# Kernel optimization log

Measured on AMD Instinct MI355X. Metric: run time of the kernel, lower is better.

Reference implementation:

```python
import jax, jax.numpy as jnp
import numpy as np
from jax import lax

V_PATCH_NUMS = (1, 2, 4, 8, 16)
BETA = 0.25
QUANT_RESI = 0.5
NUM_PHI = 4  # share_quant_resi=4 -> PhiPartiallyShared

# PhiPartiallyShared tick lookup (K=4 -> linspace(1/12, 11/12, 4))
def _phi_indices():
    K = NUM_PHI
    ticks = np.linspace(1/3/K, 1 - 1/3/K, K) if K == 4 else np.linspace(1/2/K, 1 - 1/2/K, K)
    SN = len(V_PATCH_NUMS)
    return [int(np.argmin(np.abs(ticks - si/(SN-1)))) for si in range(SN)]

PHI_IDX = _phi_indices()  # [0, 1, 1, 2, 3]


def phi_apply(h, w, b, ratio=QUANT_RESI):
    # h_out = (1-a)*h + a*Conv3x3(h), padding=1
    conv = lax.conv_general_dilated(h, w, (1, 1), 'SAME',
                                    dimension_numbers=('NCHW', 'OIHW', 'NCHW'))
    conv = conv + b[None, :, None, None]
    return h * (1.0 - ratio) + conv * ratio


def vq_forward(f_BChw, emb_w, phi_w, phi_b):
    f = f_BChw.astype(jnp.float32)
    B, C, H, W = f.shape
    f_ng = lax.stop_gradient(f)
    f_rest = f_ng
    f_hat = jnp.zeros_like(f)
    SN = len(V_PATCH_NUMS)
    loss = jnp.float32(0.0)
    emb_ng = lax.stop_gradient(emb_w)  # distances use .data (no grad)
    e_sq = jnp.sum(emb_ng * emb_ng, axis=1)  # [V]
    for si, pn in enumerate(V_PATCH_NUMS):
        if si != SN - 1:
            k = H // pn  # exact area pooling (divisible sizes)
            z = f_rest.reshape(B, C, pn, k, pn, k).mean(axis=(3, 5))
        else:
            z = f_rest
        z_NC = z.transpose(0, 2, 3, 1).reshape(-1, C)  # [B*pn*pn, C]
        # squared L2 distance to every code, argmin
        d = (jnp.sum(z_NC * z_NC, axis=1, keepdims=True) + e_sq
             - 2.0 * z_NC @ emb_ng.T)  # [N, V]
        idx = jnp.argmin(d, axis=1)  # [N]
        h = emb_w[idx].reshape(B, pn, pn, C).transpose(0, 3, 1, 2)  # [B,C,pn,pn]
        if si != SN - 1:
            h = jax.image.resize(h, (B, C, H, W), method='cubic')  # bicubic upsample
        pi = PHI_IDX[si]
        h = phi_apply(h, phi_w[pi], phi_b[pi])
        f_hat = f_hat + h
        f_rest = f_rest - h
        loss = loss + (BETA * jnp.mean((lax.stop_gradient(f_hat) - f) ** 2)
                       + jnp.mean((f_hat - f_ng) ** 2))
    loss = loss / SN
    # straight-through estimator
    f_hat_out = lax.stop_gradient(f_hat) - f_ng + f
    return f_hat_out, loss


def setup_inputs() -> dict:
    key = jax.random.key(0)
    k1, k2, k3 = jax.random.split(key, 3)
    B, C, H, W = 64, 32, 16, 16
    V = 4096
    f_BChw = jax.random.normal(k1, (B, C, H, W), dtype=jnp.float32)
    emb_w = jax.random.normal(k2, (V, C), dtype=jnp.float32) * 0.5
    phi_w = jax.random.normal(k3, (NUM_PHI, C, C, 3, 3), dtype=jnp.float32) * 0.05
    phi_b = jnp.zeros((NUM_PHI, C), dtype=jnp.float32)
    return {'f_BChw': f_BChw, 'emb_w': emb_w, 'phi_w': phi_w, 'phi_b': phi_b}


def reference(f_BChw, emb_w, phi_w, phi_b):
    return vq_forward(f_BChw, emb_w, phi_w, phi_b)
```

## Files before the change

kernel.cpp:

```cpp
#include <hip/hip_runtime.h>

typedef unsigned long long u64;

#define B_ 64
#define C_ 32
#define H_ 16
#define W_ 16
#define V_ 4096
#define NELEM_ (B_*C_*H_*W_)
#define NPOS_TOTAL 21824


__device__ __forceinline__ float keys_cubic(float x) {
  if (x >= 2.f) return 0.f;
  if (x >= 1.f) return ((-0.5f*x + 2.5f)*x - 4.f)*x + 2.f;
  return (1.5f*x - 2.5f)*x*x + 1.f;
}

__device__ __forceinline__ u64 pack_key(float d, int idx) {
  unsigned bu = __float_as_uint(d);
  unsigned m = bu ^ ((bu >> 31) ? 0xFFFFFFFFu : 0x80000000u);
  return ((u64)m << 32) | (unsigned)idx;
}


__global__ void setup_kernel(const float* __restrict__ f, const float* __restrict__ emb,
                             float* __restrict__ e_sq, u64* __restrict__ part,
                             float* __restrict__ z0) {
  int i = blockIdx.x*blockDim.x + threadIdx.x;
  if (i < NPOS_TOTAL) part[i] = ~0ull;
  if (i < V_) {
    const float4* p = (const float4*)(emb + (size_t)i*32);
    float s = 0.f;
#pragma unroll
    for (int j = 0; j < 8; ++j) { float4 q = p[j]; s += q.x*q.x + q.y*q.y + q.z*q.z + q.w*q.w; }
    e_sq[i] = s;
  }
  if (i < B_*C_) {
    const float4* p = (const float4*)(f + (size_t)i*256);
    float s = 0.f;
    for (int j = 0; j < 64; ++j) { float4 q = p[j]; s += (q.x + q.y) + (q.z + q.w); }
    z0[i] = s * (1.f/256.f);
  }
}


template<int P, int TILE>
__global__ void __launch_bounds__(256, 2) argmin2_kernel(
    const float* __restrict__ z, const float* __restrict__ emb,
    const float* __restrict__ e_sq, u64* __restrict__ part, int cpc) {
  __shared__ float cl[TILE*32];
  __shared__ float es[TILE];
  const int tid = threadIdx.x;
  const int n0 = blockIdx.x*(256*P) + tid;
  float zb[P][32]; float zz[P];
#pragma unroll
  for (int p = 0; p < P; ++p) {
    const float4* zp = (const float4*)(z + (size_t)(n0 + p*256)*32);
#pragma unroll
    for (int i = 0; i < 8; ++i) {
      float4 q = zp[i];
      zb[p][4*i+0]=q.x; zb[p][4*i+1]=q.y; zb[p][4*i+2]=q.z; zb[p][4*i+3]=q.w;
    }
    float s = 0.f;
#pragma unroll
    for (int i = 0; i < 32; ++i) s = fmaf(zb[p][i], zb[p][i], s);
    zz[p] = s;
  }
  const int v0 = blockIdx.y * cpc;
  float bd[P]; int bi[P];
#pragma unroll
  for (int p = 0; p < P; ++p) { bd[p] = 3.4e38f; bi[p] = v0; }
  for (int t0 = 0; t0 < cpc; t0 += TILE) {
    __syncthreads();
    const float4* src = (const float4*)(emb + (size_t)(v0 + t0)*32);
    for (int e = tid; e < TILE*8; e += 256) ((float4*)cl)[e] = src[e];
    if (tid < TILE) es[tid] = e_sq[v0 + t0 + tid];
    __syncthreads();
#pragma unroll 2
    for (int c = 0; c < TILE; ++c) {
      const float4* cp = (const float4*)(cl + c*32);
      float4 q[8];
#pragma unroll
      for (int i = 0; i < 8; ++i) q[i] = cp[i];
      float ev = es[c];
#pragma unroll
      for (int p = 0; p < P; ++p) {
        float a0=0.f, a1=0.f, a2=0.f, a3=0.f;
#pragma unroll
        for (int i = 0; i < 8; ++i) {
          a0 = fmaf(zb[p][4*i+0], q[i].x, a0);
          a1 = fmaf(zb[p][4*i+1], q[i].y, a1);
          a2 = fmaf(zb[p][4*i+2], q[i].z, a2);
          a3 = fmaf(zb[p][4*i+3], q[i].w, a3);
        }
        float dot = (a0+a1)+(a2+a3);
        float d = (zz[p] + ev) - 2.f*dot;
        bool lt = d < bd[p];
        bd[p] = lt ? d : bd[p];
        bi[p] = lt ? (v0 + t0 + c) : bi[p];
      }
    }
  }
#pragma unroll
  for (int p = 0; p < P; ++p)
    atomicMin(part + n0 + p*256, pack_key(bd[p], bi[p]));
}

__global__ void __launch_bounds__(256) argmin0_kernel(
    const float* __restrict__ z, const float* __restrict__ emb,
    const float* __restrict__ e_sq, u64* __restrict__ part) {
  __shared__ float cl[64*32];
  __shared__ float es[64];
  const int tid = threadIdx.x;
  const int v0 = blockIdx.x * 64;
  const float4* src = (const float4*)(emb + (size_t)v0*32);
  for (int e = tid; e < 64*8; e += 256) ((float4*)cl)[e] = src[e];
  if (tid < 64) es[tid] = e_sq[v0 + tid];
  __syncthreads();
  const int p = tid & 63, sub = tid >> 6;
  float zb[32];
  const float4* zp = (const float4*)(z + (size_t)p*32);
#pragma unroll
  for (int i = 0; i < 8; ++i) {
    float4 q = zp[i];
    zb[4*i+0]=q.x; zb[4*i+1]=q.y; zb[4*i+2]=q.z; zb[4*i+3]=q.w;
  }
  float zz = 0.f;
#pragma unroll
  for (int i = 0; i < 32; ++i) zz = fmaf(zb[i], zb[i], zz);
  float bd = 3.4e38f; int bi = v0;
  for (int c = sub*16; c < sub*16 + 16; ++c) {
    const float4* cp = (const float4*)(cl + c*32);
    float4 q[8];
#pragma unroll
    for (int i = 0; i < 8; ++i) q[i] = cp[i];
    float a0=0.f, a1=0.f, a2=0.f, a3=0.f;
#pragma unroll
    for (int i = 0; i < 8; ++i) {
      a0 = fmaf(zb[4*i+0], q[i].x, a0);
      a1 = fmaf(zb[4*i+1], q[i].y, a1);
      a2 = fmaf(zb[4*i+2], q[i].z, a2);
      a3 = fmaf(zb[4*i+3], q[i].w, a3);
    }
    float dot = (a0+a1)+(a2+a3);
    float d = (zz + es[c]) - 2.f*dot;
    if (d < bd) { bd = d; bi = v0 + c; }
  }
  atomicMin(part + p, pack_key(bd, bi));
}


template<int PN, int NEXT_PN, bool FIRST>
__global__ void __launch_bounds__(512) upconv_kernel(
    const u64* __restrict__ part_s,
    const float* __restrict__ emb,
    const float* __restrict__ phi_w,
    const float* __restrict__ phi_b,
    const float* __restrict__ f,
    float* __restrict__ f_hat,
    float* __restrict__ f_rest,
    float* __restrict__ z_next,
    float* __restrict__ loss_part)
{
  constexpr int PN2 = PN*PN;
  constexpr bool POOLED = (NEXT_PN != 0 && NEXT_PN < 16);
  const int b = blockIdx.x;
  const int cg = blockIdx.y;
  const int tid = threadIdx.x;

  __shared__ int   idx_s[PN2];
  __shared__ float W4[16][4];
  __shared__ int   I0[16];
  __shared__ float tmp_s[(PN < 16) ? C_*PN*16 : 1];
  __shared__ float pool_s[POOLED ? 8*256 : 1];
  union HupHs { float hup[C_*16*18]; float hs[C_*16*18]; };
  __shared__ HupHs u;
  __shared__ float wsum[8];

  for (int p = tid; p < PN2; p += 512)
    idx_s[p] = (int)(part_s[b*PN2 + p] & 0xFFFFFFFFull);

  if (PN < 16 && tid < 16) {
    float sf = (tid + 0.5f) * ((float)PN/16.f) - 0.5f;
    int i0 = (int)floorf(sf) - 1;
    float w[4]; float tot = 0.f;
#pragma unroll
    for (int t = 0; t < 4; ++t) {
      int i = i0 + t;
      float wv = (i >= 0 && i < PN) ? keys_cubic(fabsf(sf - (float)i)) : 0.f;
      w[t] = wv; tot += wv;
    }
    float r = 1.f/tot;
#pragma unroll
    for (int t = 0; t < 4; ++t) W4[tid][t] = w[t]*r;
    I0[tid] = i0;
  }
  __syncthreads();

  if (PN < 16) {
    for (int e = tid; e < C_*PN2; e += 512) {
      int c = e / PN2, p = e % PN2;
      u.hs[c*PN2 + p] = emb[(size_t)idx_s[p]*32 + c];
    }
  } else {
    for (int e = tid; e < C_*256; e += 512) {
      int c = e >> 8, p = e & 255;
      int y = p >> 4, x = p & 15;
      u.hup[(c*16 + y)*18 + 1 + x] = emb[(size_t)idx_s[p]*32 + c];
    }
    for (int e = tid; e < C_*16; e += 512) { u.hup[e*18] = 0.f; u.hup[e*18 + 17] = 0.f; }
  }
  __syncthreads();

  if (PN < 16) {
    for (int e = tid; e < C_*PN*16; e += 512) {
      int jx = e & 15; int rest = e >> 4;
      int iy = rest % PN; int c = rest / PN;
      int i0 = I0[jx];
      float s = 0.f;
#pragma unroll
      for (int t = 0; t < 4; ++t) {
        int ix = i0 + t; int ixc = min(max(ix, 0), PN-1);
        s += W4[jx][t] * u.hs[(c*PN + iy)*PN + ixc];
      }
      tmp_s[(c*PN + iy)*16 + jx] = s;
    }
    __syncthreads();
    for (int e = tid; e < C_*16; e += 512) { u.hup[e*18] = 0.f; u.hup[e*18 + 17] = 0.f; }
    for (int e = tid; e < C_*256; e += 512) {
      int jx = e & 15; int jy = (e >> 4) & 15; int c = e >> 8;
      int i0 = I0[jy];
      float s = 0.f;
#pragma unroll
      for (int t = 0; t < 4; ++t) {
        int iy = i0 + t; int iyc = min(max(iy, 0), PN-1);
        s += W4[jy][t] * tmp_s[(c*PN + iyc)*16 + jx];
      }
      u.hup[(c*16 + jy)*18 + 1 + jx] = s;
    }
    __syncthreads();
  }

  const int px = tid & 255;
  const int g  = tid >> 8;
  const int y  = px >> 4, x = px & 15;
  const int co0 = cg*8 + g*4;
  const float* wbase = phi_w + (size_t)co0*32*9;
  float acc[4];
#pragma unroll
  for (int o = 0; o < 4; ++o) acc[o] = phi_b[co0 + o];
  for (int ci = 0; ci < 32; ++ci) {
    float wn[9];
#pragma unroll
    for (int ky = 0; ky < 3; ++ky) {
      int yy = y + ky - 1;
      bool v = (yy >= 0 && yy <= 15);
      const float* r = &u.hup[(ci*16 + (v ? yy : 0))*18 + x];
      wn[ky*3+0] = v ? r[0] : 0.f;
      wn[ky*3+1] = v ? r[1] : 0.f;
      wn[ky*3+2] = v ? r[2] : 0.f;
    }
#pragma unroll
    for (int o = 0; o < 4; ++o) {
      const float* wp = wbase + ((size_t)o*32 + ci)*9;
#pragma unroll
      for (int t = 0; t < 9; ++t) acc[o] = fmaf(wp[t], wn[t], acc[o]);
    }
  }

  float lsum = 0.f;
#pragma unroll
  for (int o = 0; o < 4; ++o) {
    int co = co0 + o;
    float hv = 0.5f*u.hup[(co*16 + y)*18 + 1 + x] + 0.5f*acc[o];
    size_t gi = (((size_t)b*C_ + co)*16 + y)*16 + x;
    float fv = f[gi];
    float fh = FIRST ? hv : (f_hat[gi] + hv);
    f_hat[gi] = fh;
    if constexpr (NEXT_PN != 0) {
      float nfr = FIRST ? (fv - hv) : (f_rest[gi] - hv);
      f_rest[gi] = nfr;
      if constexpr (NEXT_PN == 16) {
        z_next[((size_t)b*256 + px)*32 + co] = nfr;
      } else {
        pool_s[(g*4 + o)*256 + px] = nfr;
      }
    }
    float dd = fh - fv;
    lsum = fmaf(dd, dd, lsum);
  }
  if constexpr (POOLED) {
    constexpr int NP = (NEXT_PN > 0) ? NEXT_PN : 1;
    constexpr int NP2 = NP*NP;
    constexpr int KP = 16/NP;
    __syncthreads();
    if (tid < 8*NP2) {
      int c_l = tid / NP2, p = tid % NP2;
      int yy = (p / NP)*KP, xx = (p % NP)*KP;
      float s = 0.f;
      for (int a = 0; a < KP; ++a)
        for (int e = 0; e < KP; ++e)
          s += pool_s[c_l*256 + (yy + a)*16 + xx + e];
      z_next[((size_t)b*NP2 + p)*32 + cg*8 + c_l] = s * (1.f/(float)(KP*KP));
    }
  }
#pragma unroll
  for (int off = 32; off > 0; off >>= 1) lsum += __shfl_down(lsum, off);
  if ((tid & 63) == 0) wsum[tid >> 6] = lsum;
  __syncthreads();
  if (tid == 0) {
    float s = 0.f;
#pragma unroll
    for (int i = 0; i < 8; ++i) s += wsum[i];
    loss_part[blockIdx.y*64 + blockIdx.x] = s;
  }
}

__global__ void loss_kernel(const float* __restrict__ loss_part, float* __restrict__ out_loss) {
  __shared__ float s[256];
  int t = threadIdx.x;
  float v = 0.f;
#pragma unroll
  for (int i = 0; i < 5; ++i) v += loss_part[i*256 + t];
  s[t] = v;
  __syncthreads();
  for (int off = 128; off > 0; off >>= 1) {
    if (t < off) s[t] += s[t + off];
    __syncthreads();
  }
  if (t == 0) out_loss[0] = s[0] * (1.25f / (5.f * (float)NELEM_));
}


extern "C" void kernel_launch(void* const* d_in, const int* in_sizes, int n_in,
                              void* d_out, int out_size, void* d_ws, size_t ws_size,
                              hipStream_t stream) {
  const float* f     = (const float*)d_in[0];
  const float* emb   = (const float*)d_in[1];
  const float* phi_w = (const float*)d_in[2];
  const float* phi_b = (const float*)d_in[3];
  float* f_hat    = (float*)d_out;
  float* out_loss = f_hat + NELEM_;

  char* ws = (char*)d_ws;
  float* f_rest = (float*)ws;
  float* z      = f_rest + NELEM_;
  u64*   part   = (u64*)(z + NELEM_);
  float* e_sq   = (float*)(part + NPOS_TOTAL);
  float* loss_part = e_sq + V_;

  const float* pw0 = phi_w;                 const float* pb0 = phi_b;
  const float* pw1 = phi_w + 1*32*32*9;     const float* pb1 = phi_b + 1*32;
  const float* pw2 = phi_w + 2*32*32*9;     const float* pb2 = phi_b + 2*32;
  const float* pw3 = phi_w + 3*32*32*9;     const float* pb3 = phi_b + 3*32;

  setup_kernel<<<(NPOS_TOTAL + 255)/256, 256, 0, stream>>>(f, emb, e_sq, part, z);

  dim3 cgrid(B_, 4);
  argmin0_kernel<<<64, 256, 0, stream>>>(z, emb, e_sq, part + 0);
  upconv_kernel<1, 2, true><<<cgrid, 512, 0, stream>>>(part + 0, emb, pw0, pb0,
      f, f_hat, f_rest, z, loss_part + 0*256);
  argmin2_kernel<1,16><<<dim3(1,256), 256, 0, stream>>>(z, emb, e_sq, part + 64, 16);
  upconv_kernel<2, 4, false><<<cgrid, 512, 0, stream>>>(part + 64, emb, pw1, pb1,
      f, f_hat, f_rest, z, loss_part + 1*256);
  argmin2_kernel<2,32><<<dim3(2,128), 256, 0, stream>>>(z, emb, e_sq, part + 320, 32);
  upconv_kernel<4, 8, false><<<cgrid, 512, 0, stream>>>(part + 320, emb, pw2, pb2,
      f, f_hat, f_rest, z, loss_part + 2*256);
  argmin2_kernel<4,64><<<dim3(4,64), 256, 0, stream>>>(z, emb, e_sq, part + 1344, 64);
  upconv_kernel<8, 16, false><<<cgrid, 512, 0, stream>>>(part + 1344, emb, pw2, pb2,
      f, f_hat, f_rest, z, loss_part + 3*256);
  argmin2_kernel<4,64><<<dim3(16,32), 256, 0, stream>>>(z, emb, e_sq, part + 5440, 128);
  upconv_kernel<16, 0, false><<<cgrid, 512, 0, stream>>>(part + 5440, emb, pw3, pb3,
      f, f_hat, f_rest, z, loss_part + 4*256);

  loss_kernel<<<1, 256, 0, stream>>>(loss_part, out_loss);
}
```

Before: 240.2 us.

## Replace atomicMin argmin with per-chunk partial keys reduced in upconv

The argmin kernels no longer stage codebook tiles in shared memory. Each thread streams code vectors straight from global memory with double-buffered register prefetch. Instead of atomicMin into a pre-cleared buffer, each codebook chunk writes its own partial key, and the following upconv kernel reduces across chunks. This removes the init pass, the atomics and the block barriers, at the cost of larger partial buffers and a serial reduction loop in upconv. The partial buffers reuse the f_rest workspace, which is safe only because f_rest is no longer written in the last pre-final stage. Grid shapes are retuned per stage.

```diff
diff --git a/kernel.cpp b/kernel.cpp
--- a/kernel.cpp
+++ b/kernel.cpp
@@ -4,11 +4,8 @@
 
 #define B_ 64
 #define C_ 32
-#define H_ 16
-#define W_ 16
 #define V_ 4096
-#define NELEM_ (B_*C_*H_*W_)
-#define NPOS_TOTAL 21824
+#define NELEM_ (B_*C_*16*16)
 
 
 __device__ __forceinline__ float keys_cubic(float x) {
@@ -25,10 +22,8 @@
 
 
 __global__ void setup_kernel(const float* __restrict__ f, const float* __restrict__ emb,
-                             float* __restrict__ e_sq, u64* __restrict__ part,
-                             float* __restrict__ z0) {
+                             float* __restrict__ e_sq, float* __restrict__ z0) {
   int i = blockIdx.x*blockDim.x + threadIdx.x;
-  if (i < NPOS_TOTAL) part[i] = ~0ull;
   if (i < V_) {
     const float4* p = (const float4*)(emb + (size_t)i*32);
     float s = 0.f;
@@ -45,12 +40,11 @@
 }
 
 
-template<int P, int TILE>
-__global__ void __launch_bounds__(256, 2) argmin2_kernel(
+template<int P>
+__global__ void __launch_bounds__(256) argmin_kernel(
     const float* __restrict__ z, const float* __restrict__ emb,
-    const float* __restrict__ e_sq, u64* __restrict__ part, int cpc) {
-  __shared__ float cl[TILE*32];
-  __shared__ float es[TILE];
+    const float* __restrict__ e_sq, u64* __restrict__ part_lo,
+    u64* __restrict__ part_hi, int split, int N, int cpc) {
   const int tid = threadIdx.x;
   const int n0 = blockIdx.x*(256*P) + tid;
   float zb[P][32]; float zz[P];
@@ -71,89 +65,148 @@
   float bd[P]; int bi[P];
 #pragma unroll
   for (int p = 0; p < P; ++p) { bd[p] = 3.4e38f; bi[p] = v0; }
-  for (int t0 = 0; t0 < cpc; t0 += TILE) {
-    __syncthreads();
-    const float4* src = (const float4*)(emb + (size_t)(v0 + t0)*32);
-    for (int e = tid; e < TILE*8; e += 256) ((float4*)cl)[e] = src[e];
-    if (tid < TILE) es[tid] = e_sq[v0 + t0 + tid];
-    __syncthreads();
-#pragma unroll 2
-    for (int c = 0; c < TILE; ++c) {
-      const float4* cp = (const float4*)(cl + c*32);
-      float4 q[8];
-#pragma unroll
-      for (int i = 0; i < 8; ++i) q[i] = cp[i];
-      float ev = es[c];
-#pragma unroll
-      for (int p = 0; p < P; ++p) {
-        float a0=0.f, a1=0.f, a2=0.f, a3=0.f;
-#pragma unroll
-        for (int i = 0; i < 8; ++i) {
-          a0 = fmaf(zb[p][4*i+0], q[i].x, a0);
-          a1 = fmaf(zb[p][4*i+1], q[i].y, a1);
-          a2 = fmaf(zb[p][4*i+2], q[i].z, a2);
-          a3 = fmaf(zb[p][4*i+3], q[i].w, a3);
-        }
-        float dot = (a0+a1)+(a2+a3);
-        float d = (zz[p] + ev) - 2.f*dot;
-        bool lt = d < bd[p];
-        bd[p] = lt ? d : bd[p];
-        bi[p] = lt ? (v0 + t0 + c) : bi[p];
-      }
-    }
-  }
-#pragma unroll
-  for (int p = 0; p < P; ++p)
-    atomicMin(part + n0 + p*256, pack_key(bd[p], bi[p]));
+
+  float4 qa[8], qb[8];
+  {
+    const float4* e4 = (const float4*)(emb + (size_t)v0*32);
+#pragma unroll
+    for (int i = 0; i < 8; ++i) qa[i] = e4[i];
+  }
+  for (int c = 0; c < cpc; c += 2) {
+    const int v = v0 + c;
+    {
+      const float4* en = (const float4*)(emb + (size_t)(v+1)*32);
+#pragma unroll
+      for (int i = 0; i < 8; ++i) qb[i] = en[i];
+    }
+    float ev = e_sq[v];
+#pragma unroll
+    for (int p = 0; p < P; ++p) {
+      float a0=0.f,a1=0.f,a2=0.f,a3=0.f;
+#pragma unroll
+      for (int i = 0; i < 8; ++i) {
+        a0 = fmaf(zb[p][4*i+0], qa[i].x, a0);
+        a1 = fmaf(zb[p][4*i+1], qa[i].y, a1);
+        a2 = fmaf(zb[p][4*i+2], qa[i].z, a2);
+        a3 = fmaf(zb[p][4*i+3], qa[i].w, a3);
+      }
+      float dot = (a0+a1)+(a2+a3);
+      float d = (zz[p] + ev) - 2.f*dot;
+      bool lt = d < bd[p];
+      bd[p] = lt ? d : bd[p];
+      bi[p] = lt ? v : bi[p];
+    }
+    int v2 = v + 2; if (v2 > V_-1) v2 = V_-1;
+    {
+      const float4* en = (const float4*)(emb + (size_t)v2*32);
+#pragma unroll
+      for (int i = 0; i < 8; ++i) qa[i] = en[i];
+    }
+    ev = e_sq[v+1];
+#pragma unroll
+    for (int p = 0; p < P; ++p) {
+      float a0=0.f,a1=0.f,a2=0.f,a3=0.f;
+#pragma unroll
+      for (int i = 0; i < 8; ++i) {
+        a0 = fmaf(zb[p][4*i+0], qb[i].x, a0);
+        a1 = fmaf(zb[p][4*i+1], qb[i].y, a1);
+        a2 = fmaf(zb[p][4*i+2], qb[i].z, a2);
+        a3 = fmaf(zb[p][4*i+3], qb[i].w, a3);
+      }
+      float dot = (a0+a1)+(a2+a3);
+      float d = (zz[p] + ev) - 2.f*dot;
+      bool lt = d < bd[p];
+      bd[p] = lt ? d : bd[p];
+      bi[p] = lt ? (v+1) : bi[p];
+    }
+  }
+  u64* pp = (blockIdx.y < split) ? (part_lo + (size_t)blockIdx.y*N)
+                                 : (part_hi + (size_t)(blockIdx.y - split)*N);
+#pragma unroll
+  for (int p = 0; p < P; ++p) pp[n0 + p*256] = pack_key(bd[p], bi[p]);
 }
 
 __global__ void __launch_bounds__(256) argmin0_kernel(
     const float* __restrict__ z, const float* __restrict__ emb,
-    const float* __restrict__ e_sq, u64* __restrict__ part) {
-  __shared__ float cl[64*32];
-  __shared__ float es[64];
-  const int tid = threadIdx.x;
-  const int v0 = blockIdx.x * 64;
-  const float4* src = (const float4*)(emb + (size_t)v0*32);
-  for (int e = tid; e < 64*8; e += 256) ((float4*)cl)[e] = src[e];
-  if (tid < 64) es[tid] = e_sq[v0 + tid];
+    const float* __restrict__ e_sq, u64* __restrict__ part_lo) {
+  __shared__ u64 wkey[4][64];
+  const int tid = threadIdx.x, lane = tid & 63;
+  const int w = __builtin_amdgcn_readfirstlane(tid >> 6);
+  float zb[32];
+  {
+    const float4* zp = (const float4*)(z + (size_t)lane*32);
+#pragma unroll
+    for (int i = 0; i < 8; ++i) {
+      float4 q = zp[i];
+      zb[4*i+0]=q.x; zb[4*i+1]=q.y; zb[4*i+2]=q.z; zb[4*i+3]=q.w;
+    }
+  }
+  float zz = 0.f;
+#pragma unroll
+  for (int i = 0; i < 32; ++i) zz = fmaf(zb[i], zb[i], zz);
+  const int v0 = blockIdx.x*256 + w*64;
+  float bd = 3.4e38f; int bi = v0;
+  float4 qa[8], qb[8];
+  {
+    const float4* e4 = (const float4*)(emb + (size_t)v0*32);
+#pragma unroll
+    for (int i = 0; i < 8; ++i) qa[i] = e4[i];
+  }
+  for (int c = 0; c < 64; c += 2) {
+    const int v = v0 + c;
+    {
+      const float4* en = (const float4*)(emb + (size_t)(v+1)*32);
+#pragma unroll
+      for (int i = 0; i < 8; ++i) qb[i] = en[i];
+    }
+    float ev = e_sq[v];
+    {
+      float a0=0.f,a1=0.f,a2=0.f,a3=0.f;
+#pragma unroll
+      for (int i = 0; i < 8; ++i) {
+        a0 = fmaf(zb[4*i+0], qa[i].x, a0);
+        a1 = fmaf(zb[4*i+1], qa[i].y, a1);
+        a2 = fmaf(zb[4*i+2], qa[i].z, a2);
+        a3 = fmaf(zb[4*i+3], qa[i].w, a3);
+      }
+      float d = (zz + ev) - 2.f*((a0+a1)+(a2+a3));
+      if (d < bd) { bd = d; bi = v; }
+    }
+    int v2 = v + 2; if (v2 > V_-1) v2 = V_-1;
+    {
+      const float4* en = (const float4*)(emb + (size_t)v2*32);
+#pragma unroll
+      for (int i = 0; i < 8; ++i) qa[i] = en[i];
+    }
+    ev = e_sq[v+1];
+    {
+      float a0=0.f,a1=0.f,a2=0.f,a3=0.f;
+#pragma unroll
+      for (int i = 0; i < 8; ++i) {
+        a0 = fmaf(zb[4*i+0], qb[i].x, a0);
+        a1 = fmaf(zb[4*i+1], qb[i].y, a1);
+        a2 = fmaf(zb[4*i+2], qb[i].z, a2);
+        a3 = fmaf(zb[4*i+3], qb[i].w, a3);
+      }
+      float d = (zz + ev) - 2.f*((a0+a1)+(a2+a3));
+      if (d < bd) { bd = d; bi = v+1; }
+    }
+  }
+  wkey[tid >> 6][lane] = pack_key(bd, bi);
   __syncthreads();
-  const int p = tid & 63, sub = tid >> 6;
-  float zb[32];
-  const float4* zp = (const float4*)(z + (size_t)p*32);
-#pragma unroll
-  for (int i = 0; i < 8; ++i) {
-    float4 q = zp[i];
-    zb[4*i+0]=q.x; zb[4*i+1]=q.y; zb[4*i+2]=q.z; zb[4*i+3]=q.w;
-  }
-  float zz = 0.f;
-#pragma unroll
-  for (int i = 0; i < 32; ++i) zz = fmaf(zb[i], zb[i], zz);
-  float bd = 3.4e38f; int bi = v0;
-  for (int c = sub*16; c < sub*16 + 16; ++c) {
-    const float4* cp = (const float4*)(cl + c*32);
-    float4 q[8];
-#pragma unroll
-    for (int i = 0; i < 8; ++i) q[i] = cp[i];
-    float a0=0.f, a1=0.f, a2=0.f, a3=0.f;
-#pragma unroll
-    for (int i = 0; i < 8; ++i) {
-      a0 = fmaf(zb[4*i+0], q[i].x, a0);
-      a1 = fmaf(zb[4*i+1], q[i].y, a1);
-      a2 = fmaf(zb[4*i+2], q[i].z, a2);
-      a3 = fmaf(zb[4*i+3], q[i].w, a3);
-    }
-    float dot = (a0+a1)+(a2+a3);
-    float d = (zz + es[c]) - 2.f*dot;
-    if (d < bd) { bd = d; bi = v0 + c; }
-  }
-  atomicMin(part + p, pack_key(bd, bi));
+  if (tid < 64) {
+    u64 best = wkey[0][tid];
+#pragma unroll
+    for (int ww = 1; ww < 4; ++ww) { u64 kk = wkey[ww][tid]; if (kk < best) best = kk; }
+    part_lo[blockIdx.x*64 + tid] = best;
+  }
 }
 
 
 template<int PN, int NEXT_PN, bool FIRST>
 __global__ void __launch_bounds__(512) upconv_kernel(
-    const u64* __restrict__ part_s,
+    const u64* __restrict__ part_lo, const u64* __restrict__ part_hi,
+    int split, int nvc,
     const float* __restrict__ emb,
     const float* __restrict__ phi_w,
     const float* __restrict__ phi_b,
@@ -164,6 +217,7 @@
     float* __restrict__ loss_part)
 {
   constexpr int PN2 = PN*PN;
+  constexpr int NPOS = B_*PN2;
   constexpr bool POOLED = (NEXT_PN != 0 && NEXT_PN < 16);
   const int b = blockIdx.x;
   const int cg = blockIdx.y;
@@ -178,8 +232,17 @@
   __shared__ HupHs u;
   __shared__ float wsum[8];
 
-  for (int p = tid; p < PN2; p += 512)
-    idx_s[p] = (int)(part_s[b*PN2 + p] & 0xFFFFFFFFull);
+  for (int p = tid; p < PN2; p += 512) {
+    int n = b*PN2 + p;
+    u64 best = ~0ull;
+    for (int vc = 0; vc < nvc; ++vc) {
+      const u64* pp = (vc < split) ? (part_lo + (size_t)vc*NPOS)
+                                   : (part_hi + (size_t)(vc - split)*NPOS);
+      u64 kk = pp[n];
+      if (kk < best) best = kk;
+    }
+    idx_s[p] = (int)(best & 0xFFFFFFFFull);
+  }
 
   if (PN < 16 && tid < 16) {
     float sf = (tid + 0.5f) * ((float)PN/16.f) - 0.5f;
@@ -280,10 +343,10 @@
     f_hat[gi] = fh;
     if constexpr (NEXT_PN != 0) {
       float nfr = FIRST ? (fv - hv) : (f_rest[gi] - hv);
-      f_rest[gi] = nfr;
       if constexpr (NEXT_PN == 16) {
         z_next[((size_t)b*256 + px)*32 + co] = nfr;
       } else {
+        f_rest[gi] = nfr;
         pool_s[(g*4 + o)*256 + px] = nfr;
       }
     }
@@ -344,35 +407,36 @@
   float* out_loss = f_hat + NELEM_;
 
   char* ws = (char*)d_ws;
-  float* f_rest = (float*)ws;
-  float* z      = f_rest + NELEM_;
-  u64*   part   = (u64*)(z + NELEM_);
-  float* e_sq   = (float*)(part + NPOS_TOTAL);
+  float* f_rest  = (float*)ws;
+  float* z       = f_rest + NELEM_;
+  u64*   part_lo = (u64*)(z + NELEM_);
+  float* e_sq    = (float*)(part_lo + 262144);
   float* loss_part = e_sq + V_;
+  u64*   part_hi = (u64*)f_rest;
 
   const float* pw0 = phi_w;                 const float* pb0 = phi_b;
   const float* pw1 = phi_w + 1*32*32*9;     const float* pb1 = phi_b + 1*32;
   const float* pw2 = phi_w + 2*32*32*9;     const float* pb2 = phi_b + 2*32;
   const float* pw3 = phi_w + 3*32*32*9;     const float* pb3 = phi_b + 3*32;
 
-  setup_kernel<<<(NPOS_TOTAL + 255)/256, 256, 0, stream>>>(f, emb, e_sq, part, z);
+  setup_kernel<<<16, 256, 0, stream>>>(f, emb, e_sq, z);
 
   dim3 cgrid(B_, 4);
-  argmin0_kernel<<<64, 256, 0, stream>>>(z, emb, e_sq, part + 0);
-  upconv_kernel<1, 2, true><<<cgrid, 512, 0, stream>>>(part + 0, emb, pw0, pb0,
-      f, f_hat, f_rest, z, loss_part + 0*256);
-  argmin2_kernel<1,16><<<dim3(1,256), 256, 0, stream>>>(z, emb, e_sq, part + 64, 16);
-  upconv_kernel<2, 4, false><<<cgrid, 512, 0, stream>>>(part + 64, emb, pw1, pb1,
-      f, f_hat, f_rest, z, loss_part + 1*256);
-  argmin2_kernel<2,32><<<dim3(2,128), 256, 0, stream>>>(z, emb, e_sq, part + 320, 32);
-  upconv_kernel<4, 8, false><<<cgrid, 512, 0, stream>>>(part + 320, emb, pw2, pb2,
-      f, f_hat, f_rest, z, loss_part + 2*256);
-  argmin2_kernel<4,64><<<dim3(4,64), 256, 0, stream>>>(z, emb, e_sq, part + 1344, 64);
-  upconv_kernel<8, 16, false><<<cgrid, 512, 0, stream>>>(part + 1344, emb, pw2, pb2,
-      f, f_hat, f_rest, z, loss_part + 3*256);
-  argmin2_kernel<4,64><<<dim3(16,32), 256, 0, stream>>>(z, emb, e_sq, part + 5440, 128);
-  upconv_kernel<16, 0, false><<<cgrid, 512, 0, stream>>>(part + 5440, emb, pw3, pb3,
-      f, f_hat, f_rest, z, loss_part + 4*256);
+  argmin0_kernel<<<16, 256, 0, stream>>>(z, emb, e_sq, part_lo);
+  upconv_kernel<1, 2, true><<<cgrid, 512, 0, stream>>>(part_lo, part_hi, 64, 16,
+      emb, pw0, pb0, f, f_hat, f_rest, z, loss_part + 0*256);
+  argmin_kernel<1><<<dim3(1,32), 256, 0, stream>>>(z, emb, e_sq, part_lo, part_hi, 64, 256, 128);
+  upconv_kernel<2, 4, false><<<cgrid, 512, 0, stream>>>(part_lo, part_hi, 64, 32,
+      emb, pw1, pb1, f, f_hat, f_rest, z, loss_part + 1*256);
+  argmin_kernel<2><<<dim3(2,64), 256, 0, stream>>>(z, emb, e_sq, part_lo, part_hi, 64, 1024, 64);
+  upconv_kernel<4, 8, false><<<cgrid, 512, 0, stream>>>(part_lo, part_hi, 64, 64,
+      emb, pw2, pb2, f, f_hat, f_rest, z, loss_part + 2*256);
+  argmin_kernel<2><<<dim3(8,64), 256, 0, stream>>>(z, emb, e_sq, part_lo, part_hi, 64, 4096, 64);
+  upconv_kernel<8, 16, false><<<cgrid, 512, 0, stream>>>(part_lo, part_hi, 64, 64,
+      emb, pw2, pb2, f, f_hat, f_rest, z, loss_part + 3*256);
+  argmin_kernel<4><<<dim3(16,32), 256, 0, stream>>>(z, emb, e_sq, part_lo, part_hi, 16, 16384, 128);
+  upconv_kernel<16, 0, false><<<cgrid, 512, 0, stream>>>(part_lo, part_hi, 16, 32,
+      emb, pw3, pb3, f, f_hat, f_rest, z, loss_part + 4*256);
 
   loss_kernel<<<1, 256, 0, stream>>>(loss_part, out_loss);
 }
```

New measurement: 340.0 us. 41.6% more time.

## Replace global atomicMin argmin merging with per-chunk partial buffers reduced in upconv

Applied to the files above, without the earlier changes.

Argmin kernels now write each codebook chunk's packed best key to a dedicated partial slot instead of using global 64-bit atomicMin, and upconv reduces these partials in shared memory before decoding indices. This removes the atomic contention and the initialisation pass over the partial buffer in setup. The last stage reuses the now-unneeded f_rest region as extra partial storage, so f_rest writes are skipped when the next stage reads z directly. argmin0 is also restructured to read codes straight from global memory, and the stage-1 argmin tile changes. The cost is more memory traffic for the partials and an extra reduction step at the start of every upconv.

```diff
diff --git a/kernel.cpp b/kernel.cpp
--- a/kernel.cpp
+++ b/kernel.cpp
@@ -4,11 +4,8 @@
 
 #define B_ 64
 #define C_ 32
-#define H_ 16
-#define W_ 16
 #define V_ 4096
-#define NELEM_ (B_*C_*H_*W_)
-#define NPOS_TOTAL 21824
+#define NELEM_ (B_*C_*16*16)
 
 
 __device__ __forceinline__ float keys_cubic(float x) {
@@ -25,10 +22,8 @@
 
 
 __global__ void setup_kernel(const float* __restrict__ f, const float* __restrict__ emb,
-                             float* __restrict__ e_sq, u64* __restrict__ part,
-                             float* __restrict__ z0) {
+                             float* __restrict__ e_sq, float* __restrict__ z0) {
   int i = blockIdx.x*blockDim.x + threadIdx.x;
-  if (i < NPOS_TOTAL) part[i] = ~0ull;
   if (i < V_) {
     const float4* p = (const float4*)(emb + (size_t)i*32);
     float s = 0.f;
@@ -48,7 +43,8 @@
 template<int P, int TILE>
 __global__ void __launch_bounds__(256, 2) argmin2_kernel(
     const float* __restrict__ z, const float* __restrict__ emb,
-    const float* __restrict__ e_sq, u64* __restrict__ part, int cpc) {
+    const float* __restrict__ e_sq, u64* __restrict__ part_lo,
+    u64* __restrict__ part_hi, int split, int N, int cpc) {
   __shared__ float cl[TILE*32];
   __shared__ float es[TILE];
   const int tid = threadIdx.x;
@@ -102,40 +98,39 @@
       }
     }
   }
-#pragma unroll
-  for (int p = 0; p < P; ++p)
-    atomicMin(part + n0 + p*256, pack_key(bd[p], bi[p]));
+  u64* pp = (blockIdx.y < split) ? (part_lo + (size_t)blockIdx.y*N)
+                                 : (part_hi + (size_t)(blockIdx.y - split)*N);
+#pragma unroll
+  for (int p = 0; p < P; ++p) pp[n0 + p*256] = pack_key(bd[p], bi[p]);
 }
 
 __global__ void __launch_bounds__(256) argmin0_kernel(
     const float* __restrict__ z, const float* __restrict__ emb,
-    const float* __restrict__ e_sq, u64* __restrict__ part) {
-  __shared__ float cl[64*32];
-  __shared__ float es[64];
-  const int tid = threadIdx.x;
-  const int v0 = blockIdx.x * 64;
-  const float4* src = (const float4*)(emb + (size_t)v0*32);
-  for (int e = tid; e < 64*8; e += 256) ((float4*)cl)[e] = src[e];
-  if (tid < 64) es[tid] = e_sq[v0 + tid];
-  __syncthreads();
-  const int p = tid & 63, sub = tid >> 6;
+    const float* __restrict__ e_sq, u64* __restrict__ part_lo) {
+  __shared__ u64 wkey[4][64];
+  const int tid = threadIdx.x, lane = tid & 63;
+  const int w = tid >> 6;
   float zb[32];
-  const float4* zp = (const float4*)(z + (size_t)p*32);
-#pragma unroll
-  for (int i = 0; i < 8; ++i) {
-    float4 q = zp[i];
-    zb[4*i+0]=q.x; zb[4*i+1]=q.y; zb[4*i+2]=q.z; zb[4*i+3]=q.w;
+  {
+    const float4* zp = (const float4*)(z + (size_t)lane*32);
+#pragma unroll
+    for (int i = 0; i < 8; ++i) {
+      float4 q = zp[i];
+      zb[4*i+0]=q.x; zb[4*i+1]=q.y; zb[4*i+2]=q.z; zb[4*i+3]=q.w;
+    }
   }
   float zz = 0.f;
 #pragma unroll
   for (int i = 0; i < 32; ++i) zz = fmaf(zb[i], zb[i], zz);
+  const int v0 = blockIdx.x*256 + w*64;
   float bd = 3.4e38f; int bi = v0;
-  for (int c = sub*16; c < sub*16 + 16; ++c) {
-    const float4* cp = (const float4*)(cl + c*32);
+  for (int c = 0; c < 64; ++c) {
+    const int v = v0 + c;
+    const float4* e4 = (const float4*)(emb + (size_t)v*32);
     float4 q[8];
 #pragma unroll
-    for (int i = 0; i < 8; ++i) q[i] = cp[i];
-    float a0=0.f, a1=0.f, a2=0.f, a3=0.f;
+    for (int i = 0; i < 8; ++i) q[i] = e4[i];
+    float a0=0.f,a1=0.f,a2=0.f,a3=0.f;
 #pragma unroll
     for (int i = 0; i < 8; ++i) {
       a0 = fmaf(zb[4*i+0], q[i].x, a0);
@@ -143,17 +138,24 @@
       a2 = fmaf(zb[4*i+2], q[i].z, a2);
       a3 = fmaf(zb[4*i+3], q[i].w, a3);
     }
-    float dot = (a0+a1)+(a2+a3);
-    float d = (zz + es[c]) - 2.f*dot;
-    if (d < bd) { bd = d; bi = v0 + c; }
-  }
-  atomicMin(part + p, pack_key(bd, bi));
+    float d = (zz + e_sq[v]) - 2.f*((a0+a1)+(a2+a3));
+    if (d < bd) { bd = d; bi = v; }
+  }
+  wkey[w][lane] = pack_key(bd, bi);
+  __syncthreads();
+  if (tid < 64) {
+    u64 best = wkey[0][tid];
+#pragma unroll
+    for (int ww = 1; ww < 4; ++ww) { u64 kk = wkey[ww][tid]; if (kk < best) best = kk; }
+    part_lo[blockIdx.x*64 + tid] = best;
+  }
 }
 
 
 template<int PN, int NEXT_PN, bool FIRST>
 __global__ void __launch_bounds__(512) upconv_kernel(
-    const u64* __restrict__ part_s,
+    const u64* __restrict__ part_lo, const u64* __restrict__ part_hi,
+    int split, int nvc,
     const float* __restrict__ emb,
     const float* __restrict__ phi_w,
     const float* __restrict__ phi_b,
@@ -164,11 +166,14 @@
     float* __restrict__ loss_part)
 {
   constexpr int PN2 = PN*PN;
+  constexpr int NPOS = B_*PN2;
+  constexpr int S = 512/PN2 < 1 ? 1 : 512/PN2;
   constexpr bool POOLED = (NEXT_PN != 0 && NEXT_PN < 16);
   const int b = blockIdx.x;
   const int cg = blockIdx.y;
   const int tid = threadIdx.x;
 
+  __shared__ u64   red[512];
   __shared__ int   idx_s[PN2];
   __shared__ float W4[16][4];
   __shared__ int   I0[16];
@@ -178,8 +183,29 @@
   __shared__ HupHs u;
   __shared__ float wsum[8];
 
-  for (int p = tid; p < PN2; p += 512)
-    idx_s[p] = (int)(part_s[b*PN2 + p] & 0xFFFFFFFFull);
+  {
+    const int p = tid % PN2;
+    const int s = tid / PN2;
+    const int n = b*PN2 + p;
+    u64 best = ~0ull;
+    for (int vc = s; vc < nvc; vc += S) {
+      const u64* pp = (vc < split) ? (part_lo + (size_t)vc*NPOS)
+                                   : (part_hi + (size_t)(vc - split)*NPOS);
+      u64 kk = pp[n];
+      if (kk < best) best = kk;
+    }
+    red[tid] = best;
+    __syncthreads();
+#pragma unroll
+    for (int h = S/2; h > 0; h >>= 1) {
+      if (tid < h*PN2) {
+        u64 o = red[tid + h*PN2];
+        if (o < red[tid]) red[tid] = o;
+      }
+      __syncthreads();
+    }
+    if (tid < PN2) idx_s[tid] = (int)(red[tid] & 0xFFFFFFFFull);
+  }
 
   if (PN < 16 && tid < 16) {
     float sf = (tid + 0.5f) * ((float)PN/16.f) - 0.5f;
@@ -280,10 +306,10 @@
     f_hat[gi] = fh;
     if constexpr (NEXT_PN != 0) {
       float nfr = FIRST ? (fv - hv) : (f_rest[gi] - hv);
-      f_rest[gi] = nfr;
       if constexpr (NEXT_PN == 16) {
         z_next[((size_t)b*256 + px)*32 + co] = nfr;
       } else {
+        f_rest[gi] = nfr;
         pool_s[(g*4 + o)*256 + px] = nfr;
       }
     }
@@ -344,35 +370,36 @@
   float* out_loss = f_hat + NELEM_;
 
   char* ws = (char*)d_ws;
-  float* f_rest = (float*)ws;
-  float* z      = f_rest + NELEM_;
-  u64*   part   = (u64*)(z + NELEM_);
-  float* e_sq   = (float*)(part + NPOS_TOTAL);
+  float* f_rest  = (float*)ws;
+  float* z       = f_rest + NELEM_;
+  u64*   part_lo = (u64*)(z + NELEM_);
+  float* e_sq    = (float*)(part_lo + 262144);
   float* loss_part = e_sq + V_;
+  u64*   part_hi = (u64*)f_rest;
 
   const float* pw0 = phi_w;                 const float* pb0 = phi_b;
   const float* pw1 = phi_w + 1*32*32*9;     const float* pb1 = phi_b + 1*32;
   const float* pw2 = phi_w + 2*32*32*9;     const float* pb2 = phi_b + 2*32;
   const float* pw3 = phi_w + 3*32*32*9;     const float* pb3 = phi_b + 3*32;
 
-  setup_kernel<<<(NPOS_TOTAL + 255)/256, 256, 0, stream>>>(f, emb, e_sq, part, z);
+  setup_kernel<<<16, 256, 0, stream>>>(f, emb, e_sq, z);
 
   dim3 cgrid(B_, 4);
-  argmin0_kernel<<<64, 256, 0, stream>>>(z, emb, e_sq, part + 0);
-  upconv_kernel<1, 2, true><<<cgrid, 512, 0, stream>>>(part + 0, emb, pw0, pb0,
-      f, f_hat, f_rest, z, loss_part + 0*256);
-  argmin2_kernel<1,16><<<dim3(1,256), 256, 0, stream>>>(z, emb, e_sq, part + 64, 16);
-  upconv_kernel<2, 4, false><<<cgrid, 512, 0, stream>>>(part + 64, emb, pw1, pb1,
-      f, f_hat, f_rest, z, loss_part + 1*256);
-  argmin2_kernel<2,32><<<dim3(2,128), 256, 0, stream>>>(z, emb, e_sq, part + 320, 32);
-  upconv_kernel<4, 8, false><<<cgrid, 512, 0, stream>>>(part + 320, emb, pw2, pb2,
-      f, f_hat, f_rest, z, loss_part + 2*256);
-  argmin2_kernel<4,64><<<dim3(4,64), 256, 0, stream>>>(z, emb, e_sq, part + 1344, 64);
-  upconv_kernel<8, 16, false><<<cgrid, 512, 0, stream>>>(part + 1344, emb, pw2, pb2,
-      f, f_hat, f_rest, z, loss_part + 3*256);
-  argmin2_kernel<4,64><<<dim3(16,32), 256, 0, stream>>>(z, emb, e_sq, part + 5440, 128);
-  upconv_kernel<16, 0, false><<<cgrid, 512, 0, stream>>>(part + 5440, emb, pw3, pb3,
-      f, f_hat, f_rest, z, loss_part + 4*256);
+  argmin0_kernel<<<16, 256, 0, stream>>>(z, emb, e_sq, part_lo);
+  upconv_kernel<1, 2, true><<<cgrid, 512, 0, stream>>>(part_lo, part_hi, 64, 16,
+      emb, pw0, pb0, f, f_hat, f_rest, z, loss_part + 0*256);
+  argmin2_kernel<1,32><<<dim3(1,128), 256, 0, stream>>>(z, emb, e_sq, part_lo, part_hi, 192, 256, 32);
+  upconv_kernel<2, 4, false><<<cgrid, 512, 0, stream>>>(part_lo, part_hi, 192, 128,
+      emb, pw1, pb1, f, f_hat, f_rest, z, loss_part + 1*256);
+  argmin2_kernel<2,32><<<dim3(2,128), 256, 0, stream>>>(z, emb, e_sq, part_lo, part_hi, 192, 1024, 32);
+  upconv_kernel<4, 8, false><<<cgrid, 512, 0, stream>>>(part_lo, part_hi, 192, 128,
+      emb, pw2, pb2, f, f_hat, f_rest, z, loss_part + 2*256);
+  argmin2_kernel<4,64><<<dim3(4,64), 256, 0, stream>>>(z, emb, e_sq, part_lo, part_hi, 96, 4096, 64);
+  upconv_kernel<8, 16, false><<<cgrid, 512, 0, stream>>>(part_lo, part_hi, 96, 64,
+      emb, pw2, pb2, f, f_hat, f_rest, z, loss_part + 3*256);
+  argmin2_kernel<4,64><<<dim3(16,32), 256, 0, stream>>>(z, emb, e_sq, part_lo, part_hi, 16, 16384, 128);
+  upconv_kernel<16, 0, false><<<cgrid, 512, 0, stream>>>(part_lo, part_hi, 16, 32,
+      emb, pw3, pb3, f, f_hat, f_rest, z, loss_part + 4*256);
 
   loss_kernel<<<1, 256, 0, stream>>>(loss_part, out_loss);
 }
```

After: 268.5 us (median of 2 runs). 1.12x slower.
